# Kernel tuning notes

Hardware: AMD Instinct MI355X
Metric: run time of the kernel (lower is better)

The kernel has to match this reference:

```python
import jax, jax.numpy as jnp
import numpy as np

HIDDEN_DIM = 512  # H; hidden/encoder feature dim is 2H = 1024


def setup_inputs() -> dict:
    key = jax.random.key(0)
    k1, k2, k3, k4, k5 = jax.random.split(key, 5)
    B, S, D2, H = 16, 4096, 2 * HIDDEN_DIM, HIDDEN_DIM
    hidden = jax.random.normal(k1, (B, D2), dtype=jnp.float32)
    encoder_outputs = jax.random.normal(k2, (B, S, D2), dtype=jnp.float32)
    # nn.Linear(4H, H): weight [H, 4H] in torch; store transposed [4H, H] for x @ W
    W_attn = jax.random.normal(k3, (2 * D2, H), dtype=jnp.float32) * (1.0 / np.sqrt(2 * D2))
    b_attn = jax.random.normal(k4, (H,), dtype=jnp.float32) * 0.01
    # nn.Linear(H, 1, bias=False): weight [1, H] -> vector [H]
    w_v = jax.random.normal(k5, (H,), dtype=jnp.float32) * (1.0 / np.sqrt(H))
    return {"hidden": hidden, "encoder_outputs": encoder_outputs,
            "W_attn": W_attn, "b_attn": b_attn, "w_v": w_v}


def reference(hidden, encoder_outputs, W_attn, b_attn, w_v):
    B, S, D2 = encoder_outputs.shape
    # Broadcast decoder hidden over seq positions and concat with encoder outputs.
    hid = jnp.broadcast_to(hidden[:, None, :], (B, S, D2))
    cat = jnp.concatenate([hid, encoder_outputs], axis=2)        # [B, S, 4H]
    energy = jnp.tanh(cat @ W_attn + b_attn)                      # [B, S, H]
    scores = jnp.einsum('bsh,h->bs', energy, w_v)                 # [B, S]
    attention = jax.nn.softmax(scores, axis=1)                    # [B, S]
    context = jnp.einsum('bs,bsd->bd', attention, encoder_outputs)  # [B, 2H]
    return context
```

## Files before the change

### kernel.cpp

```cpp
#include <hip/hip_runtime.h>
#include <hip/hip_bf16.h>
#include <math.h>

#define HD   512
#define D2   1024
#define SEQ  4096
#define BAT  16
#define BM   128
#define BK   32

typedef _Float16 half8  __attribute__((ext_vector_type(8)));
typedef float    f32x4  __attribute__((ext_vector_type(4)));
typedef float    f32x16 __attribute__((ext_vector_type(16)));
typedef __attribute__((address_space(3))) void lds_void_t;
typedef __attribute__((address_space(1))) void glb_void_t;

__global__ void wconv_kernel(const float* __restrict__ W, _Float16* __restrict__ WtS) {
  const int kt = blockIdx.x;
  const int nh = blockIdx.y;
  const int t  = threadIdx.x;
  #pragma unroll
  for (int kc = 0; kc < 4; ++kc) {
    half8 h;
    #pragma unroll
    for (int j = 0; j < 8; ++j) {
      const int k = kt * 32 + (kc >> 1) * 16 + (kc & 1) * 8 + j;
      h[j] = (_Float16)W[(size_t)(D2 + k) * HD + nh * 256 + t];
    }
    *(half8*)(WtS + (((size_t)(nh * 32 + kt) * 4 + kc) * 256 + t) * 8) = h;
  }
}

__global__ void hproj_kernel(const float* __restrict__ hidden,
                             const float* __restrict__ W,
                             float* __restrict__ hproj) {
  const int b  = blockIdx.x >> 3;
  const int kc = blockIdx.x & 7;
  const int h  = threadIdx.x;
  float a0 = 0.f, a1 = 0.f;
  #pragma unroll 4
  for (int i = 0; i < 128; ++i) {
    const int d = kc * 128 + i;
    const float hd = hidden[b * D2 + d];
    a0 += hd * W[(size_t)d * HD + h];
    a1 += hd * W[(size_t)d * HD + h + 256];
  }
  atomicAdd(&hproj[b * HD + h], a0);
  atomicAdd(&hproj[b * HD + h + 256], a1);
}

__global__ __launch_bounds__(256, 2) void scores_kernel(
    const float* __restrict__ enc, const _Float16* __restrict__ WtS,
    const float* __restrict__ hproj, const float* __restrict__ b_attn,
    const float* __restrict__ w_v, float* __restrict__ scores)
{
  __shared__ __align__(16) _Float16 As[2][4 * 128 * 8];
  __shared__ __align__(16) _Float16 Bs[2][4 * 256 * 8];

  const int s0   = blockIdx.x * BM;
  const int nh   = blockIdx.y;
  const int b    = blockIdx.z;
  const int tid  = threadIdx.x, lane = tid & 63, w = tid >> 6;
  const int wy   = w >> 1, wx = w & 1;
  const int llo  = lane & 31, lhi = lane >> 5;

  const float* encB = enc + ((size_t)b * SEQ + s0) * D2;

  const int arow = tid >> 1, akh = tid & 1;
  const float* aSrc = encB + (size_t)arow * D2 + akh * 16;

  const _Float16* WtB = WtS + (size_t)nh * 32 * 8192;

  int afOff[2][2];
  #pragma unroll
  for (int mi = 0; mi < 2; ++mi)
    #pragma unroll
    for (int q = 0; q < 2; ++q)
      afOff[mi][q] = (((q * 2 + lhi) * 128) + wy * 64 + mi * 32 + llo) * 8;
  int bfOff[2][4];
  #pragma unroll
  for (int q = 0; q < 2; ++q)
    #pragma unroll
    for (int nf = 0; nf < 4; ++nf)
      bfOff[q][nf] = (((q * 2 + lhi) * 256) + wx * 128 + nf * 32 + llo) * 8;

  f32x16 acc[2][4];
  #pragma unroll
  for (int mi = 0; mi < 2; ++mi)
    #pragma unroll
    for (int nf = 0; nf < 4; ++nf)
      acc[mi][nf] = (f32x16)(0.f);

  f32x4 R[2][4];

  auto loadA = [&](int kt, f32x4* r) {
    const float* p = aSrc + kt * BK;
    r[0] = *(const f32x4*)(p);
    r[1] = *(const f32x4*)(p + 4);
    r[2] = *(const f32x4*)(p + 8);
    r[3] = *(const f32x4*)(p + 12);
  };
  auto storeA = [&](int buf, const f32x4* r) {
    half8 h0, h1;
    #pragma unroll
    for (int j = 0; j < 4; ++j) {
      h0[j] = (_Float16)r[0][j]; h0[4 + j] = (_Float16)r[1][j];
      h1[j] = (_Float16)r[2][j]; h1[4 + j] = (_Float16)r[3][j];
    }
    *(half8*)&As[buf][((akh * 2 + 0) * 128 + arow) * 8] = h0;
    *(half8*)&As[buf][((akh * 2 + 1) * 128 + arow) * 8] = h1;
  };
  auto issueB = [&](int kt, int buf) {
    #pragma unroll
    for (int i = 0; i < 4; ++i) {
      const int c = i * 256 + tid;
      __builtin_amdgcn_global_load_lds(
          (glb_void_t*)(WtB + ((size_t)kt * 1024 + c) * 8),
          (lds_void_t*)((char*)&Bs[buf][0] + c * 16), 16, 0, 0);
    }
  };

  loadA(0, R[0]);
  storeA(0, R[0]);
  issueB(0, 0);
  loadA(1, R[0]);
  loadA(2, R[1]);
  __syncthreads();

  #pragma unroll 2
  for (int kt = 0; kt < 32; ++kt) {
    const int cur = kt & 1, nxt = cur ^ 1;
    if (kt + 1 < 32) { storeA(nxt, R[cur]); issueB(kt + 1, nxt); }
    if (kt + 3 < 32) loadA(kt + 3, R[cur]);
    half8 af[2][2], bf[2][4];
    #pragma unroll
    for (int mi = 0; mi < 2; ++mi)
      #pragma unroll
      for (int q = 0; q < 2; ++q)
        af[mi][q] = *(const half8*)&As[cur][afOff[mi][q]];
    #pragma unroll
    for (int q = 0; q < 2; ++q)
      #pragma unroll
      for (int nf = 0; nf < 4; ++nf)
        bf[q][nf] = *(const half8*)&Bs[cur][bfOff[q][nf]];
    #pragma unroll
    for (int nf = 0; nf < 4; ++nf)
      #pragma unroll
      for (int mi = 0; mi < 2; ++mi)
        #pragma unroll
        for (int q = 0; q < 2; ++q)
          acc[mi][nf] = __builtin_amdgcn_mfma_f32_32x32x16_f16(af[mi][q], bf[q][nf], acc[mi][nf], 0, 0, 0);
    __syncthreads();
  }

  float p[2][16];
  #pragma unroll
  for (int mi = 0; mi < 2; ++mi)
    #pragma unroll
    for (int r = 0; r < 16; ++r) p[mi][r] = 0.f;

  #pragma unroll
  for (int nf = 0; nf < 4; ++nf) {
    const int n = nh * 256 + wx * 128 + nf * 32 + llo;
    const float hb = hproj[b * HD + n] + b_attn[n];
    const float wv = w_v[n];
    #pragma unroll
    for (int mi = 0; mi < 2; ++mi)
      #pragma unroll
      for (int r = 0; r < 16; ++r) {
        float x = fminf(fmaxf(acc[mi][nf][r] + hb, -15.f), 15.f);
        float ex = __expf(2.f * x);
        p[mi][r] += wv * __fdividef(ex - 1.f, ex + 1.f);
      }
  }
  #pragma unroll
  for (int off = 1; off <= 16; off <<= 1)
    #pragma unroll
    for (int mi = 0; mi < 2; ++mi)
      #pragma unroll
      for (int r = 0; r < 16; ++r)
        p[mi][r] += __shfl_xor(p[mi][r], off, 64);

  if (llo == 0) {
    #pragma unroll
    for (int mi = 0; mi < 2; ++mi)
      #pragma unroll
      for (int r = 0; r < 16; ++r) {
        const int m = wy * 64 + mi * 32 + (r & 3) + 8 * (r >> 2) + 4 * lhi;
        atomicAdd(&scores[b * SEQ + s0 + m], p[mi][r]);
      }
  }
}

__global__ void softmax_kernel(float* __restrict__ scores) {
  const int b = blockIdx.x;
  float* sc = scores + b * SEQ;
  __shared__ float red[16];
  const int tid = threadIdx.x;
  float loc[16];
  float mx = -1e30f;
  #pragma unroll
  for (int i = 0; i < 16; ++i) { loc[i] = sc[i * 256 + tid]; mx = fmaxf(mx, loc[i]); }
  #pragma unroll
  for (int off = 32; off >= 1; off >>= 1) mx = fmaxf(mx, __shfl_xor(mx, off, 64));
  if ((tid & 63) == 0) red[tid >> 6] = mx;
  __syncthreads();
  mx = fmaxf(fmaxf(red[0], red[1]), fmaxf(red[2], red[3]));
  float sum = 0.f;
  #pragma unroll
  for (int i = 0; i < 16; ++i) { loc[i] = __expf(loc[i] - mx); sum += loc[i]; }
  #pragma unroll
  for (int off = 32; off >= 1; off >>= 1) sum += __shfl_xor(sum, off, 64);
  if ((tid & 63) == 0) red[8 + (tid >> 6)] = sum;
  __syncthreads();
  sum = red[8] + red[9] + red[10] + red[11];
  const float inv = 1.0f / sum;
  #pragma unroll
  for (int i = 0; i < 16; ++i) sc[i * 256 + tid] = loc[i] * inv;
}

__global__ __launch_bounds__(256) void context_kernel(const float* __restrict__ attn,
                                                      const float* __restrict__ enc,
                                                      float* __restrict__ out) {
  const int b  = blockIdx.y;
  const int s0 = blockIdx.x * 64;
  const int tid = threadIdx.x;
  const float* encB = enc + ((size_t)b * SEQ + s0) * D2 + tid * 4;
  const float* at   = attn + b * SEQ + s0;
  f32x4 acc0 = {0.f, 0.f, 0.f, 0.f}, acc1 = {0.f, 0.f, 0.f, 0.f};
  #pragma unroll 8
  for (int i = 0; i < 64; i += 2) {
    acc0 += at[i]     * *(const f32x4*)(encB + (size_t)i * D2);
    acc1 += at[i + 1] * *(const f32x4*)(encB + (size_t)(i + 1) * D2);
  }
  f32x4 acc = acc0 + acc1;
  float* o = out + b * D2 + tid * 4;
  atomicAdd(o + 0, acc[0]);
  atomicAdd(o + 1, acc[1]);
  atomicAdd(o + 2, acc[2]);
  atomicAdd(o + 3, acc[3]);
}

extern "C" void kernel_launch(void* const* d_in, const int* in_sizes, int n_in,
                              void* d_out, int out_size, void* d_ws, size_t ws_size,
                              hipStream_t stream) {
  (void)in_sizes; (void)n_in; (void)ws_size;
  const float* hidden = (const float*)d_in[0];
  const float* enc    = (const float*)d_in[1];
  const float* W      = (const float*)d_in[2];
  const float* b_attn = (const float*)d_in[3];
  const float* w_v    = (const float*)d_in[4];
  float* out = (float*)d_out;

  char* ws = (char*)d_ws;
  _Float16* WtS = (_Float16*)ws;
  float* hproj  = (float*)(ws + (1 << 20));
  float* scores = (float*)(ws + (1 << 20) + 32768);

  hipMemsetAsync(d_out, 0, (size_t)out_size * sizeof(float), stream);
  hipMemsetAsync(hproj, 0, BAT * HD * sizeof(float), stream);
  hipMemsetAsync(scores, 0, (size_t)BAT * SEQ * sizeof(float), stream);

  wconv_kernel  <<<dim3(32, 2),             256, 0, stream>>>(W, WtS);
  hproj_kernel  <<<dim3(128),               256, 0, stream>>>(hidden, W, hproj);
  scores_kernel <<<dim3(SEQ / BM, 2, BAT),  256, 0, stream>>>(enc, WtS, hproj, b_attn, w_v, scores);
  softmax_kernel<<<dim3(BAT),               256, 0, stream>>>(scores);
  context_kernel<<<dim3(SEQ / 64, BAT),     256, 0, stream>>>(scores, enc, out);
}
```

Before: 496.3 us.

## Fuse scores, softmax and context into one kernel with deferred normalization

Measured after the change: 508.7 us. 2.5% more time.

```diff
diff --git a/kernel.cpp b/kernel.cpp
--- a/kernel.cpp
+++ b/kernel.cpp
@@ -6,8 +6,6 @@
 #define D2   1024
 #define SEQ  4096
 #define BAT  16
-#define BM   128
-#define BK   32
 
 typedef _Float16 half8  __attribute__((ext_vector_type(8)));
 typedef float    f32x4  __attribute__((ext_vector_type(4)));
@@ -17,18 +15,18 @@
 
 __global__ void wconv_kernel(const float* __restrict__ W, _Float16* __restrict__ WtS) {
   const int kt = blockIdx.x;
-  const int nh = blockIdx.y;
   const int t  = threadIdx.x;
   #pragma unroll
-  for (int kc = 0; kc < 4; ++kc) {
-    half8 h;
-    #pragma unroll
-    for (int j = 0; j < 8; ++j) {
-      const int k = kt * 32 + (kc >> 1) * 16 + (kc & 1) * 8 + j;
-      h[j] = (_Float16)W[(size_t)(D2 + k) * HD + nh * 256 + t];
-    }
-    *(half8*)(WtS + (((size_t)(nh * 32 + kt) * 4 + kc) * 256 + t) * 8) = h;
-  }
+  for (int kc = 0; kc < 4; ++kc)
+    #pragma unroll
+    for (int nn = 0; nn < 2; ++nn) {
+      const int n = nn * 256 + t;
+      half8 h;
+      #pragma unroll
+      for (int j = 0; j < 8; ++j)
+        h[j] = (_Float16)W[(size_t)(D2 + kt * 32 + kc * 8 + j) * HD + n];
+      *(half8*)(WtS + ((size_t)(kt * 4 + kc) * 512 + n) * 8) = h;
+    }
 }
 
 __global__ void hproj_kernel(const float* __restrict__ hidden,
@@ -49,40 +47,27 @@
   atomicAdd(&hproj[b * HD + h + 256], a1);
 }
 
-__global__ __launch_bounds__(256, 2) void scores_kernel(
+__global__ __launch_bounds__(512, 2) void fused_kernel(
     const float* __restrict__ enc, const _Float16* __restrict__ WtS,
     const float* __restrict__ hproj, const float* __restrict__ b_attn,
-    const float* __restrict__ w_v, float* __restrict__ scores)
+    const float* __restrict__ w_v, float* __restrict__ ctx,
+    float* __restrict__ sumexp)
 {
   __shared__ __align__(16) _Float16 As[2][4 * 128 * 8];
-  __shared__ __align__(16) _Float16 Bs[2][4 * 256 * 8];
-
-  const int s0   = blockIdx.x * BM;
-  const int nh   = blockIdx.y;
-  const int b    = blockIdx.z;
-  const int tid  = threadIdx.x, lane = tid & 63, w = tid >> 6;
-  const int wy   = w >> 1, wx = w & 1;
-  const int llo  = lane & 31, lhi = lane >> 5;
+  __shared__ __align__(16) _Float16 Bs[2][4 * 512 * 8];
+  __shared__ float s_sc[128];
+  __shared__ float s_w[128];
+
+  const int s0  = blockIdx.x * 128;
+  const int b   = blockIdx.y;
+  const int tid = threadIdx.x, lane = tid & 63, w = tid >> 6;
+  const int wy  = w >> 2, wx = w & 3;
+  const int llo = lane & 31, lhi = lane >> 5;
 
   const float* encB = enc + ((size_t)b * SEQ + s0) * D2;
 
-  const int arow = tid >> 1, akh = tid & 1;
-  const float* aSrc = encB + (size_t)arow * D2 + akh * 16;
-
-  const _Float16* WtB = WtS + (size_t)nh * 32 * 8192;
-
-  int afOff[2][2];
-  #pragma unroll
-  for (int mi = 0; mi < 2; ++mi)
-    #pragma unroll
-    for (int q = 0; q < 2; ++q)
-      afOff[mi][q] = (((q * 2 + lhi) * 128) + wy * 64 + mi * 32 + llo) * 8;
-  int bfOff[2][4];
-  #pragma unroll
-  for (int q = 0; q < 2; ++q)
-    #pragma unroll
-    for (int nf = 0; nf < 4; ++nf)
-      bfOff[q][nf] = (((q * 2 + lhi) * 256) + wx * 128 + nf * 32 + llo) * 8;
+  const int arow = tid >> 2, akc = tid & 3;
+  const float* aSrc = encB + (size_t)arow * D2 + akc * 8;
 
   f32x16 acc[2][4];
   #pragma unroll
@@ -91,66 +76,71 @@
     for (int nf = 0; nf < 4; ++nf)
       acc[mi][nf] = (f32x16)(0.f);
 
-  f32x4 R[2][4];
-
-  auto loadA = [&](int kt, f32x4* r) {
-    const float* p = aSrc + kt * BK;
-    r[0] = *(const f32x4*)(p);
-    r[1] = *(const f32x4*)(p + 4);
-    r[2] = *(const f32x4*)(p + 8);
-    r[3] = *(const f32x4*)(p + 12);
-  };
-  auto storeA = [&](int buf, const f32x4* r) {
-    half8 h0, h1;
+  f32x4 R[2][2];
+
+  auto loadA = [&](int kt, int slot) {
+    const float* p = aSrc + kt * 32;
+    R[slot][0] = *(const f32x4*)(p);
+    R[slot][1] = *(const f32x4*)(p + 4);
+  };
+  auto storeA = [&](int buf, int slot) {
+    half8 h;
     #pragma unroll
     for (int j = 0; j < 4; ++j) {
-      h0[j] = (_Float16)r[0][j]; h0[4 + j] = (_Float16)r[1][j];
-      h1[j] = (_Float16)r[2][j]; h1[4 + j] = (_Float16)r[3][j];
-    }
-    *(half8*)&As[buf][((akh * 2 + 0) * 128 + arow) * 8] = h0;
-    *(half8*)&As[buf][((akh * 2 + 1) * 128 + arow) * 8] = h1;
+      h[j] = (_Float16)R[slot][0][j]; h[4 + j] = (_Float16)R[slot][1][j];
+    }
+    *(half8*)&As[buf][(akc * 128 + arow) * 8] = h;
   };
   auto issueB = [&](int kt, int buf) {
     #pragma unroll
     for (int i = 0; i < 4; ++i) {
-      const int c = i * 256 + tid;
+      const int c = i * 512 + tid;
       __builtin_amdgcn_global_load_lds(
-          (glb_void_t*)(WtB + ((size_t)kt * 1024 + c) * 8),
+          (glb_void_t*)(WtS + ((size_t)kt * 2048 + c) * 8),
           (lds_void_t*)((char*)&Bs[buf][0] + c * 16), 16, 0, 0);
     }
   };
-
-  loadA(0, R[0]);
-  storeA(0, R[0]);
+  auto compute = [&](int cur) {
+    #pragma unroll
+    for (int q = 0; q < 2; ++q) {
+      half8 aq[2], bq[4];
+      #pragma unroll
+      for (int mi = 0; mi < 2; ++mi)
+        aq[mi] = *(const half8*)&As[cur][((q * 2 + lhi) * 128 + wy * 64 + mi * 32 + llo) * 8];
+      #pragma unroll
+      for (int nf = 0; nf < 4; ++nf)
+        bq[nf] = *(const half8*)&Bs[cur][((q * 2 + lhi) * 512 + wx * 128 + nf * 32 + llo) * 8];
+      #pragma unroll
+      for (int nf = 0; nf < 4; ++nf)
+        #pragma unroll
+        for (int mi = 0; mi < 2; ++mi)
+          acc[mi][nf] = __builtin_amdgcn_mfma_f32_32x32x16_f16(aq[mi], bq[nf], acc[mi][nf], 0, 0, 0);
+    }
+  };
+  auto step = [&](int kt, int cur) {
+    const int nxt = cur ^ 1;
+    if (kt + 1 < 32) issueB(kt + 1, nxt);
+    __builtin_amdgcn_sched_barrier(0);
+    if (kt + 1 < 32) storeA(nxt, nxt);
+    if (kt + 3 < 32) loadA(kt + 3, nxt);
+    compute(cur);
+    if (kt < 29)
+      asm volatile("s_waitcnt vmcnt(2) lgkmcnt(0)\n\ts_barrier" ::: "memory");
+    else
+      asm volatile("s_waitcnt vmcnt(0) lgkmcnt(0)\n\ts_barrier" ::: "memory");
+  };
+
+  if (tid < 128) s_sc[tid] = 0.f;
   issueB(0, 0);
-  loadA(1, R[0]);
-  loadA(2, R[1]);
-  __syncthreads();
-
-  #pragma unroll 2
-  for (int kt = 0; kt < 32; ++kt) {
-    const int cur = kt & 1, nxt = cur ^ 1;
-    if (kt + 1 < 32) { storeA(nxt, R[cur]); issueB(kt + 1, nxt); }
-    if (kt + 3 < 32) loadA(kt + 3, R[cur]);
-    half8 af[2][2], bf[2][4];
-    #pragma unroll
-    for (int mi = 0; mi < 2; ++mi)
-      #pragma unroll
-      for (int q = 0; q < 2; ++q)
-        af[mi][q] = *(const half8*)&As[cur][afOff[mi][q]];
-    #pragma unroll
-    for (int q = 0; q < 2; ++q)
-      #pragma unroll
-      for (int nf = 0; nf < 4; ++nf)
-        bf[q][nf] = *(const half8*)&Bs[cur][bfOff[q][nf]];
-    #pragma unroll
-    for (int nf = 0; nf < 4; ++nf)
-      #pragma unroll
-      for (int mi = 0; mi < 2; ++mi)
-        #pragma unroll
-        for (int q = 0; q < 2; ++q)
-          acc[mi][nf] = __builtin_amdgcn_mfma_f32_32x32x16_f16(af[mi][q], bf[q][nf], acc[mi][nf], 0, 0, 0);
-    __syncthreads();
+  loadA(0, 0);
+  storeA(0, 0);
+  loadA(1, 1);
+  loadA(2, 0);
+  asm volatile("s_waitcnt lgkmcnt(0)\n\ts_barrier" ::: "memory");
+
+  for (int kt2 = 0; kt2 < 16; ++kt2) {
+    step(2 * kt2,     0);
+    step(2 * kt2 + 1, 1);
   }
 
   float p[2][16];
@@ -161,7 +151,7 @@
 
   #pragma unroll
   for (int nf = 0; nf < 4; ++nf) {
-    const int n = nh * 256 + wx * 128 + nf * 32 + llo;
+    const int n = wx * 128 + nf * 32 + llo;
     const float hb = hproj[b * HD + n] + b_attn[n];
     const float wv = w_v[n];
     #pragma unroll
@@ -187,64 +177,56 @@
       #pragma unroll
       for (int r = 0; r < 16; ++r) {
         const int m = wy * 64 + mi * 32 + (r & 3) + 8 * (r >> 2) + 4 * lhi;
-        atomicAdd(&scores[b * SEQ + s0 + m], p[mi][r]);
+        atomicAdd(&s_sc[m], p[mi][r]);
       }
   }
-}
-
-__global__ void softmax_kernel(float* __restrict__ scores) {
-  const int b = blockIdx.x;
-  float* sc = scores + b * SEQ;
-  __shared__ float red[16];
-  const int tid = threadIdx.x;
-  float loc[16];
-  float mx = -1e30f;
-  #pragma unroll
-  for (int i = 0; i < 16; ++i) { loc[i] = sc[i * 256 + tid]; mx = fmaxf(mx, loc[i]); }
-  #pragma unroll
-  for (int off = 32; off >= 1; off >>= 1) mx = fmaxf(mx, __shfl_xor(mx, off, 64));
-  if ((tid & 63) == 0) red[tid >> 6] = mx;
   __syncthreads();
-  mx = fmaxf(fmaxf(red[0], red[1]), fmaxf(red[2], red[3]));
-  float sum = 0.f;
-  #pragma unroll
-  for (int i = 0; i < 16; ++i) { loc[i] = __expf(loc[i] - mx); sum += loc[i]; }
-  #pragma unroll
-  for (int off = 32; off >= 1; off >>= 1) sum += __shfl_xor(sum, off, 64);
-  if ((tid & 63) == 0) red[8 + (tid >> 6)] = sum;
+
+  if (tid < 128) s_w[tid] = __expf(s_sc[tid]);
   __syncthreads();
-  sum = red[8] + red[9] + red[10] + red[11];
-  const float inv = 1.0f / sum;
-  #pragma unroll
-  for (int i = 0; i < 16; ++i) sc[i * 256 + tid] = loc[i] * inv;
-}
-
-__global__ __launch_bounds__(256) void context_kernel(const float* __restrict__ attn,
-                                                      const float* __restrict__ enc,
-                                                      float* __restrict__ out) {
-  const int b  = blockIdx.y;
-  const int s0 = blockIdx.x * 64;
-  const int tid = threadIdx.x;
-  const float* encB = enc + ((size_t)b * SEQ + s0) * D2 + tid * 4;
-  const float* at   = attn + b * SEQ + s0;
-  f32x4 acc0 = {0.f, 0.f, 0.f, 0.f}, acc1 = {0.f, 0.f, 0.f, 0.f};
-  #pragma unroll 8
-  for (int i = 0; i < 64; i += 2) {
-    acc0 += at[i]     * *(const f32x4*)(encB + (size_t)i * D2);
-    acc1 += at[i + 1] * *(const f32x4*)(encB + (size_t)(i + 1) * D2);
-  }
-  f32x4 acc = acc0 + acc1;
-  float* o = out + b * D2 + tid * 4;
-  atomicAdd(o + 0, acc[0]);
-  atomicAdd(o + 1, acc[1]);
-  atomicAdd(o + 2, acc[2]);
-  atomicAdd(o + 3, acc[3]);
+  if (tid < 64) {
+    float v = s_w[tid] + s_w[tid + 64];
+    #pragma unroll
+    for (int off = 32; off >= 1; off >>= 1) v += __shfl_xor(v, off, 64);
+    if (tid == 0) atomicAdd(&sumexp[b], v);
+  }
+
+  const int tg = tid >> 7, cb = (tid & 127) * 8;
+  const float* pr = encB + (size_t)tg * 32 * D2 + cb;
+  const float* wp = &s_w[tg * 32];
+  f32x4 c0a = {0.f,0.f,0.f,0.f}, c0b = {0.f,0.f,0.f,0.f};
+  f32x4 c1a = {0.f,0.f,0.f,0.f}, c1b = {0.f,0.f,0.f,0.f};
+  #pragma unroll 4
+  for (int i = 0; i < 32; i += 2) {
+    const float w0 = wp[i], w1 = wp[i + 1];
+    c0a += w0 * *(const f32x4*)(pr + (size_t)i * D2);
+    c0b += w0 * *(const f32x4*)(pr + (size_t)i * D2 + 4);
+    c1a += w1 * *(const f32x4*)(pr + (size_t)(i + 1) * D2);
+    c1b += w1 * *(const f32x4*)(pr + (size_t)(i + 1) * D2 + 4);
+  }
+  c0a += c1a; c0b += c1b;
+  float* cp = ctx + b * D2 + cb;
+  #pragma unroll
+  for (int j = 0; j < 4; ++j) {
+    atomicAdd(cp + j,     c0a[j]);
+    atomicAdd(cp + 4 + j, c0b[j]);
+  }
+}
+
+__global__ void norm_kernel(const float* __restrict__ ctx,
+                            const float* __restrict__ sumexp,
+                            float* __restrict__ out) {
+  const int b = blockIdx.x, t = threadIdx.x;
+  const float inv = 1.0f / sumexp[b];
+  f32x4 v = *(const f32x4*)(ctx + b * D2 + t * 4);
+  v *= inv;
+  *(f32x4*)(out + b * D2 + t * 4) = v;
 }
 
 extern "C" void kernel_launch(void* const* d_in, const int* in_sizes, int n_in,
                               void* d_out, int out_size, void* d_ws, size_t ws_size,
                               hipStream_t stream) {
-  (void)in_sizes; (void)n_in; (void)ws_size;
+  (void)in_sizes; (void)n_in; (void)ws_size; (void)out_size;
   const float* hidden = (const float*)d_in[0];
   const float* enc    = (const float*)d_in[1];
   const float* W      = (const float*)d_in[2];
@@ -255,15 +237,15 @@
   char* ws = (char*)d_ws;
   _Float16* WtS = (_Float16*)ws;
   float* hproj  = (float*)(ws + (1 << 20));
-  float* scores = (float*)(ws + (1 << 20) + 32768);
-
-  hipMemsetAsync(d_out, 0, (size_t)out_size * sizeof(float), stream);
-  hipMemsetAsync(hproj, 0, BAT * HD * sizeof(float), stream);
-  hipMemsetAsync(scores, 0, (size_t)BAT * SEQ * sizeof(float), stream);
-
-  wconv_kernel  <<<dim3(32, 2),             256, 0, stream>>>(W, WtS);
-  hproj_kernel  <<<dim3(128),               256, 0, stream>>>(hidden, W, hproj);
-  scores_kernel <<<dim3(SEQ / BM, 2, BAT),  256, 0, stream>>>(enc, WtS, hproj, b_attn, w_v, scores);
-  softmax_kernel<<<dim3(BAT),               256, 0, stream>>>(scores);
-  context_kernel<<<dim3(SEQ / 64, BAT),     256, 0, stream>>>(scores, enc, out);
-}
+  float* ctx    = (float*)(ws + (1 << 20) + 32768);
+  float* sumexp = (float*)(ws + (1 << 20) + 32768 + 65536);
+
+  hipMemsetAsync(hproj,  0, BAT * HD * sizeof(float), stream);
+  hipMemsetAsync(ctx,    0, BAT * D2 * sizeof(float), stream);
+  hipMemsetAsync(sumexp, 0, BAT * sizeof(float), stream);
+
+  wconv_kernel <<<dim3(32),           256, 0, stream>>>(W, WtS);
+  hproj_kernel <<<dim3(128),          256, 0, stream>>>(hidden, W, hproj);
+  fused_kernel <<<dim3(SEQ / 128, BAT), 512, 0, stream>>>(enc, WtS, hproj, b_attn, w_v, ctx, sumexp);
+  norm_kernel  <<<dim3(BAT),          256, 0, stream>>>(ctx, sumexp, out);
+}
```
